# Kernel optimization log

Hardware: AMD Instinct MI355X
Metric: run time of the kernel (lower is better)

Reference implementation:

```python
import jax, jax.numpy as jnp
import numpy as np

H = 2048        # hidden_size
NH = 16         # num q heads
NKV = 4         # num kv heads
HD = 128        # head_dim
G = NH // NKV   # GQA group size
B = 32          # batch (decode sequences)
S = 4096        # max kv cache length per sequence
SCALE = HD ** -0.5
NEG = -1e30


def setup_inputs() -> dict:
    key = jax.random.key(0)
    ks = jax.random.split(key, 6)
    hidden_states = jax.random.normal(ks[0], (B, 1, H), dtype=jnp.float32)
    kv_cache = jax.random.normal(ks[1], (B, S, 2, NKV, HD), dtype=jnp.float32)
    seq_lens = jax.random.randint(ks[2], (B,), 1, S, dtype=jnp.int32)
    slot_mapping = seq_lens - 1  # write current token's k/v at its slot
    positions = (seq_lens - 1)[:, None].astype(jnp.int32)
    Wqkv = jax.random.normal(ks[3], (H, (NH + 2 * NKV) * HD), dtype=jnp.float32) * (H ** -0.5)
    bqkv = jax.random.normal(ks[4], ((NH + 2 * NKV) * HD,), dtype=jnp.float32) * 0.02
    Wo = jax.random.normal(ks[5], (NH * HD, H), dtype=jnp.float32) * ((NH * HD) ** -0.5)
    return {"hidden_states": hidden_states, "positions": positions, "kv_cache": kv_cache,
            "slot_mapping": slot_mapping, "seq_lens": seq_lens,
            "Wqkv": Wqkv, "bqkv": bqkv, "Wo": Wo}


def reference(hidden_states, positions, kv_cache, slot_mapping, seq_lens, Wqkv, bqkv, Wo):
    b, t, _ = hidden_states.shape  # t == 1 (decode)
    qkv = hidden_states.reshape(b * t, H) @ Wqkv + bqkv          # [B, (NH+2NKV)*HD]
    q, k, v = jnp.split(qkv, [NH * HD, (NH + NKV) * HD], axis=-1)
    q = q.reshape(b, NKV, G, HD)                                  # grouped-query layout
    k = k.reshape(b, NKV, HD)
    v = v.reshape(b, NKV, HD)
    # scatter current-step k/v into the paged cache at slot_mapping
    rows = jnp.arange(b)
    cache = kv_cache.at[rows, slot_mapping, 0].set(k)
    cache = cache.at[rows, slot_mapping, 1].set(v)
    keys = cache[:, :, 0]   # [B, S, NKV, HD]
    vals = cache[:, :, 1]   # [B, S, NKV, HD]
    # attention scores with ragged seq_lens mask
    scores = jnp.einsum('bkgd,bskd->bkgs', q, keys) * SCALE       # [B, NKV, G, S]
    valid = (jnp.arange(S)[None, :] < seq_lens[:, None])          # [B, S]
    scores = jnp.where(valid[:, None, None, :], scores, NEG)
    probs = jax.nn.softmax(scores, axis=-1)
    out = jnp.einsum('bkgs,bskd->bkgd', probs, vals)              # [B, NKV, G, HD]
    out = out.reshape(b * t, NH * HD)
    return (out @ Wo).reshape(b, t, H)
```

## Files before the change

### kernel.cpp

```cpp
#include <hip/hip_runtime.h>
#include <cstddef>

#define HQ 2048
#define NKVH 4
#define HDIM 128
#define QKV_N 3072
#define ATT_SCALE 0.08838834764831845f
#define KSPLIT 16
#define CHUNK 128
#define NCH 32

__device__ __forceinline__ float4 f4max(float4 a, float4 b) {
  return make_float4(fmaxf(a.x, b.x), fmaxf(a.y, b.y), fmaxf(a.z, b.z), fmaxf(a.w, b.w));
}

template <int N>
__global__ __launch_bounds__(256) void proj_kernel(const float* __restrict__ X,
                                                   const float* __restrict__ W,
                                                   float* __restrict__ part) {
  __shared__ union {
    float x[32][128];
    float red[32][4][64];
  } sm;
  const int t = threadIdx.x;
  const int c0 = blockIdx.x << 6;
  const int ksb = blockIdx.y;
  const int k0 = ksb << 7;
  const int c = t & 63;
  const int ksub = t >> 6;

#pragma unroll
  for (int i = 0; i < 4; ++i) {
    const int id = t + (i << 8);
    const int bb = id >> 5, kk = (id & 31) << 2;
    *reinterpret_cast<float4*>(&sm.x[bb][kk]) =
        *reinterpret_cast<const float4*>(X + bb * HQ + k0 + kk);
  }
  __syncthreads();

  float acc[32];
#pragma unroll
  for (int b = 0; b < 32; ++b) acc[b] = 0.f;

#pragma unroll
  for (int kk4 = 0; kk4 < 8; ++kk4) {
    const int kk = (ksub << 5) + (kk4 << 2);
    const float* wp = W + (size_t)(k0 + kk) * N + c0 + c;
    const float w0 = wp[0];
    const float w1 = wp[N];
    const float w2 = wp[2 * N];
    const float w3 = wp[3 * N];
#pragma unroll
    for (int b = 0; b < 32; ++b) {
      const float4 x4 = *reinterpret_cast<const float4*>(&sm.x[b][kk]);
      acc[b] = fmaf(x4.x, w0, acc[b]);
      acc[b] = fmaf(x4.y, w1, acc[b]);
      acc[b] = fmaf(x4.z, w2, acc[b]);
      acc[b] = fmaf(x4.w, w3, acc[b]);
    }
  }
  __syncthreads();
#pragma unroll
  for (int b = 0; b < 32; ++b) sm.red[b][ksub][c] = acc[b];
  __syncthreads();
#pragma unroll
  for (int i = 0; i < 8; ++i) {
    const int o = t + (i << 8);
    const int b = o >> 6, cc = o & 63;
    const float v = sm.red[b][0][cc] + sm.red[b][1][cc] + sm.red[b][2][cc] + sm.red[b][3][cc];
    part[(size_t)(ksb * 32 + b) * N + c0 + cc] = v;
  }
}

template <int NCOL, bool HAS_BIAS>
__global__ __launch_bounds__(256) void reduce_kernel(const float* __restrict__ part,
                                                     const float* __restrict__ bias,
                                                     float* __restrict__ out) {
  const int o = blockIdx.x * 256 + threadIdx.x;
  constexpr int total = 32 * NCOL;
  float s = 0.f;
#pragma unroll
  for (int ks = 0; ks < KSPLIT; ++ks) s += part[(size_t)ks * total + o];
  if (HAS_BIAS) s += bias[o % NCOL];
  out[o] = s;
}

__global__ __launch_bounds__(256, 2) void attn_kernel(const float* __restrict__ cache,
                                                      const int* __restrict__ seq_lens,
                                                      const int* __restrict__ slot_map,
                                                      const float* __restrict__ qkv,
                                                      float* __restrict__ ml,
                                                      float* __restrict__ accp) {
  __shared__ float pt[CHUNK][4];
  __shared__ float pvbuf[4][128][4];
  __shared__ float redm[4][4];
  __shared__ float redl[4][4];

  const int t = threadIdx.x;
  const int bid = blockIdx.x;
  const int chunk = bid & 31;
  const int kvh = (bid >> 5) & 3;
  const int b = bid >> 7;
  const int L = seq_lens[b];
  const int start = chunk << 7;
  if (start >= L) return;
  const int n = min(CHUNK, L - start);
  const int send = start + n;
  const int slot = slot_map[b];
  const float* __restrict__ qrow = qkv + b * QKV_N;
  const float* __restrict__ knew = qrow + 2048 + (kvh << 7);
  const float* __restrict__ vnew = qrow + 2560 + (kvh << 7);

  const int w = t >> 6, l = t & 63;
  const int l16 = l & 15, rq = l >> 4;
  const int wbase = w << 5;

  auto krow_ptr = [&](int r) -> const float* {
    int sg = start + r;
    sg = (sg < send) ? sg : start;
    return (sg == slot) ? knew : cache + (((size_t)((b << 12) + sg)) << 10) + (kvh << 7);
  };
  auto vrow_ptr = [&](int r) -> const float* {
    int sg = start + r;
    sg = (sg < send) ? sg : start;
    return (sg == slot) ? vnew : cache + (((size_t)((b << 12) + sg)) << 10) + 512 + (kvh << 7);
  };

  auto kload = [&](int st, float4* dst) {
#pragma unroll
    for (int rg = 0; rg < 4; ++rg) {
      const float* kp = krow_ptr(wbase + (st << 4) + (rg << 2) + rq) + (l16 << 3);
      dst[2 * rg] = *reinterpret_cast<const float4*>(kp);
      dst[2 * rg + 1] = *reinterpret_cast<const float4*>(kp + 4);
    }
  };
  auto vload = [&](int vt, float2* dst) {
#pragma unroll
    for (int s = 0; s < 16; ++s)
      dst[s] = *reinterpret_cast<const float2*>(vrow_ptr(wbase + (vt << 4) + s) + (l << 1));
  };

  float4 ka[8], kb[8];
  float2 va[16], vb[16];
  kload(0, ka);

  float4 qr[4][2];
#pragma unroll
  for (int g = 0; g < 4; ++g) {
#pragma unroll
    for (int e = 0; e < 2; ++e)
      qr[g][e] = *reinterpret_cast<const float4*>(qrow + ((kvh << 2) + g) * HDIM +
                                                  (l16 << 3) + (e << 2));
  }
  kload(1, kb);
  vload(0, va);
  vload(1, vb);

  float4 m4 = make_float4(-1e30f, -1e30f, -1e30f, -1e30f);
  auto score_st = [&](int st, const float4* kr) {
#pragma unroll
    for (int rg = 0; rg < 4; ++rg) {
      const float4 k0 = kr[2 * rg], k1 = kr[2 * rg + 1];
      float s0 = fmaf(k0.x, qr[0][0].x, fmaf(k0.y, qr[0][0].y, fmaf(k0.z, qr[0][0].z, k0.w * qr[0][0].w)));
      s0 = fmaf(k1.x, qr[0][1].x, fmaf(k1.y, qr[0][1].y, fmaf(k1.z, qr[0][1].z, fmaf(k1.w, qr[0][1].w, s0))));
      float s1 = fmaf(k0.x, qr[1][0].x, fmaf(k0.y, qr[1][0].y, fmaf(k0.z, qr[1][0].z, k0.w * qr[1][0].w)));
      s1 = fmaf(k1.x, qr[1][1].x, fmaf(k1.y, qr[1][1].y, fmaf(k1.z, qr[1][1].z, fmaf(k1.w, qr[1][1].w, s1))));
      float s2 = fmaf(k0.x, qr[2][0].x, fmaf(k0.y, qr[2][0].y, fmaf(k0.z, qr[2][0].z, k0.w * qr[2][0].w)));
      s2 = fmaf(k1.x, qr[2][1].x, fmaf(k1.y, qr[2][1].y, fmaf(k1.z, qr[2][1].z, fmaf(k1.w, qr[2][1].w, s2))));
      float s3 = fmaf(k0.x, qr[3][0].x, fmaf(k0.y, qr[3][0].y, fmaf(k0.z, qr[3][0].z, k0.w * qr[3][0].w)));
      s3 = fmaf(k1.x, qr[3][1].x, fmaf(k1.y, qr[3][1].y, fmaf(k1.z, qr[3][1].z, fmaf(k1.w, qr[3][1].w, s3))));
#pragma unroll
      for (int off = 1; off <= 8; off <<= 1) {
        s0 += __shfl_xor(s0, off);
        s1 += __shfl_xor(s1, off);
        s2 += __shfl_xor(s2, off);
        s3 += __shfl_xor(s3, off);
      }
      const int row = wbase + (st << 4) + (rg << 2) + rq;
      const float4 sc = make_float4(s0 * ATT_SCALE, s1 * ATT_SCALE, s2 * ATT_SCALE, s3 * ATT_SCALE);
      if (row < n) m4 = f4max(m4, sc);
      if (l16 == 0) *reinterpret_cast<float4*>(&pt[row][0]) = sc;
    }
  };

  score_st(0, ka);
  score_st(1, kb);

  m4.x = fmaxf(m4.x, __shfl_xor(m4.x, 16));
  m4.y = fmaxf(m4.y, __shfl_xor(m4.y, 16));
  m4.z = fmaxf(m4.z, __shfl_xor(m4.z, 16));
  m4.w = fmaxf(m4.w, __shfl_xor(m4.w, 16));
  m4.x = fmaxf(m4.x, __shfl_xor(m4.x, 32));
  m4.y = fmaxf(m4.y, __shfl_xor(m4.y, 32));
  m4.z = fmaxf(m4.z, __shfl_xor(m4.z, 32));
  m4.w = fmaxf(m4.w, __shfl_xor(m4.w, 32));
  if (l == 0) *reinterpret_cast<float4*>(&redm[w][0]) = m4;
  __syncthreads();
  float4 M4 = *reinterpret_cast<const float4*>(&redm[0][0]);
  M4 = f4max(M4, *reinterpret_cast<const float4*>(&redm[1][0]));
  M4 = f4max(M4, *reinterpret_cast<const float4*>(&redm[2][0]));
  M4 = f4max(M4, *reinterpret_cast<const float4*>(&redm[3][0]));

  float4 l4 = make_float4(0.f, 0.f, 0.f, 0.f);
  if (l < 32) {
    const int r = wbase + l;
    float4 e = make_float4(0.f, 0.f, 0.f, 0.f);
    if (r < n) {
      const float4 v = *reinterpret_cast<const float4*>(&pt[r][0]);
      e.x = __expf(v.x - M4.x);
      e.y = __expf(v.y - M4.y);
      e.z = __expf(v.z - M4.z);
      e.w = __expf(v.w - M4.w);
    }
    *reinterpret_cast<float4*>(&pt[r][0]) = e;
    l4 = e;
  }
#pragma unroll
  for (int off = 1; off <= 32; off <<= 1) {
    l4.x += __shfl_xor(l4.x, off);
    l4.y += __shfl_xor(l4.y, off);
    l4.z += __shfl_xor(l4.z, off);
    l4.w += __shfl_xor(l4.w, off);
  }
  if (l == 0) *reinterpret_cast<float4*>(&redl[w][0]) = l4;

  float4 accA = make_float4(0.f, 0.f, 0.f, 0.f);
  float4 accB = make_float4(0.f, 0.f, 0.f, 0.f);
#pragma unroll
  for (int s = 0; s < 16; ++s) {
    const float4 p = *reinterpret_cast<const float4*>(&pt[wbase + s][0]);
    const float2 vv = va[s];
    accA.x = fmaf(p.x, vv.x, accA.x); accA.y = fmaf(p.y, vv.x, accA.y);
    accA.z = fmaf(p.z, vv.x, accA.z); accA.w = fmaf(p.w, vv.x, accA.w);
    accB.x = fmaf(p.x, vv.y, accB.x); accB.y = fmaf(p.y, vv.y, accB.y);
    accB.z = fmaf(p.z, vv.y, accB.z); accB.w = fmaf(p.w, vv.y, accB.w);
  }
#pragma unroll
  for (int s = 0; s < 16; ++s) {
    const float4 p = *reinterpret_cast<const float4*>(&pt[wbase + 16 + s][0]);
    const float2 vv = vb[s];
    accA.x = fmaf(p.x, vv.x, accA.x); accA.y = fmaf(p.y, vv.x, accA.y);
    accA.z = fmaf(p.z, vv.x, accA.z); accA.w = fmaf(p.w, vv.x, accA.w);
    accB.x = fmaf(p.x, vv.y, accB.x); accB.y = fmaf(p.y, vv.y, accB.y);
    accB.z = fmaf(p.z, vv.y, accB.z); accB.w = fmaf(p.w, vv.y, accB.w);
  }

  *reinterpret_cast<float4*>(&pvbuf[w][l << 1][0]) = accA;
  *reinterpret_cast<float4*>(&pvbuf[w][(l << 1) + 1][0]) = accB;
  __syncthreads();

  if (t < 128) {
    const int d = t;
    float4 s0 = *reinterpret_cast<const float4*>(&pvbuf[0][d][0]);
    const float4 s1 = *reinterpret_cast<const float4*>(&pvbuf[1][d][0]);
    const float4 s2 = *reinterpret_cast<const float4*>(&pvbuf[2][d][0]);
    const float4 s3 = *reinterpret_cast<const float4*>(&pvbuf[3][d][0]);
    s0.x += s1.x + s2.x + s3.x;
    s0.y += s1.y + s2.y + s3.y;
    s0.z += s1.z + s2.z + s3.z;
    s0.w += s1.w + s2.w + s3.w;
    float* ap = accp + (size_t)bid * 512;
    ap[d] = s0.x;
    ap[128 + d] = s0.y;
    ap[256 + d] = s0.z;
    ap[384 + d] = s0.w;
  }
  if (t == 0) {
    float4 Lt = *reinterpret_cast<const float4*>(&redl[0][0]);
    const float4 l1 = *reinterpret_cast<const float4*>(&redl[1][0]);
    const float4 l2 = *reinterpret_cast<const float4*>(&redl[2][0]);
    const float4 l3 = *reinterpret_cast<const float4*>(&redl[3][0]);
    Lt.x += l1.x + l2.x + l3.x;
    Lt.y += l1.y + l2.y + l3.y;
    Lt.z += l1.z + l2.z + l3.z;
    Lt.w += l1.w + l2.w + l3.w;
    *reinterpret_cast<float4*>(ml + (size_t)bid * 8) = M4;
    *reinterpret_cast<float4*>(ml + (size_t)bid * 8 + 4) = Lt;
  }
}

__global__ __launch_bounds__(128) void combine_kernel(const int* __restrict__ seq_lens,
                                                      const float* __restrict__ ml,
                                                      const float* __restrict__ accp,
                                                      float* __restrict__ attn) {
  const int blk = blockIdx.x;
  const int g = blk & 3, kvh = (blk >> 2) & 3, b = blk >> 4;
  const int d = threadIdx.x;
  const int L = seq_lens[b];
  const int nch = (L + CHUNK - 1) >> 7;
  const int base = (b * 4 + kvh) * NCH;

  float M = -1e30f;
  for (int c = 0; c < nch; ++c) M = fmaxf(M, ml[(size_t)(base + c) * 8 + g]);
  float osum = 0.f, lsum = 0.f;
  for (int c = 0; c < nch; ++c) {
    const int idx = base + c;
    const float mc = ml[(size_t)idx * 8 + g];
    const float lc = ml[(size_t)idx * 8 + 4 + g];
    const float wgt = __expf(mc - M);
    lsum = fmaf(lc, wgt, lsum);
    osum = fmaf(wgt, accp[(size_t)idx * 512 + g * 128 + d], osum);
  }
  attn[(size_t)b * HQ + kvh * 512 + g * 128 + d] = osum / lsum;
}

extern "C" void kernel_launch(void* const* d_in, const int* in_sizes, int n_in,
                              void* d_out, int out_size, void* d_ws, size_t ws_size,
                              hipStream_t stream) {
  const float* hidden = (const float*)d_in[0];
  const float* cache = (const float*)d_in[2];
  const int* slot_map = (const int*)d_in[3];
  const int* seq_lens = (const int*)d_in[4];
  const float* Wqkv = (const float*)d_in[5];
  const float* bqkv = (const float*)d_in[6];
  const float* Wo = (const float*)d_in[7];
  float* out = (float*)d_out;
  float* ws = (float*)d_ws;

  float* qkv_part = ws;
  float* qkv      = ws + 1572864;
  float* ml       = ws + 1671168;
  float* accp     = ws + 1703936;
  float* attn     = ws + 3801088;
  float* o_part   = ws + 3866624;

  proj_kernel<QKV_N><<<dim3(48, KSPLIT), 256, 0, stream>>>(hidden, Wqkv, qkv_part);
  reduce_kernel<QKV_N, true><<<384, 256, 0, stream>>>(qkv_part, bqkv, qkv);
  attn_kernel<<<4096, 256, 0, stream>>>(cache, seq_lens, slot_map, qkv, ml, accp);
  combine_kernel<<<512, 128, 0, stream>>>(seq_lens, ml, accp, attn);
  proj_kernel<HQ><<<dim3(32, KSPLIT), 256, 0, stream>>>(attn, Wo, o_part);
  reduce_kernel<HQ, false><<<256, 256, 0, stream>>>(o_part, nullptr, out);
}
```

Baseline: 139.1 us.

## Split attention into score and PV kernels; widen projection tiles to 128 columns

The fused attention kernel is split into a score kernel, which writes scaled QK scores and per-wave maxima to workspace, and a PV kernel, which reads them back, applies exp and accumulates V. Each kernel holds fewer live registers (K or V only), so launch bounds are raised to 3 blocks per CU for higher occupancy. The extra score and max traffic through global memory, plus a second launch, is the price. Separately, the projection kernel now computes 128 columns per block with two accumulator sets, halving its grid and reusing the shared X tile across more weight columns.

```diff
diff --git a/kernel.cpp b/kernel.cpp
--- a/kernel.cpp
+++ b/kernel.cpp
@@ -23,7 +23,7 @@
     float red[32][4][64];
   } sm;
   const int t = threadIdx.x;
-  const int c0 = blockIdx.x << 6;
+  const int c0 = blockIdx.x << 7;
   const int ksb = blockIdx.y;
   const int k0 = ksb << 7;
   const int c = t & 63;
@@ -38,30 +38,35 @@
   }
   __syncthreads();
 
-  float acc[32];
-#pragma unroll
-  for (int b = 0; b < 32; ++b) acc[b] = 0.f;
+  float acc0[32], acc1[32];
+#pragma unroll
+  for (int b = 0; b < 32; ++b) { acc0[b] = 0.f; acc1[b] = 0.f; }
 
 #pragma unroll
   for (int kk4 = 0; kk4 < 8; ++kk4) {
     const int kk = (ksub << 5) + (kk4 << 2);
     const float* wp = W + (size_t)(k0 + kk) * N + c0 + c;
-    const float w0 = wp[0];
-    const float w1 = wp[N];
-    const float w2 = wp[2 * N];
-    const float w3 = wp[3 * N];
+    const float w0a = wp[0],     w0b = wp[64];
+    const float w1a = wp[N],     w1b = wp[N + 64];
+    const float w2a = wp[2 * N], w2b = wp[2 * N + 64];
+    const float w3a = wp[3 * N], w3b = wp[3 * N + 64];
 #pragma unroll
     for (int b = 0; b < 32; ++b) {
       const float4 x4 = *reinterpret_cast<const float4*>(&sm.x[b][kk]);
-      acc[b] = fmaf(x4.x, w0, acc[b]);
-      acc[b] = fmaf(x4.y, w1, acc[b]);
-      acc[b] = fmaf(x4.z, w2, acc[b]);
-      acc[b] = fmaf(x4.w, w3, acc[b]);
+      acc0[b] = fmaf(x4.x, w0a, acc0[b]);
+      acc0[b] = fmaf(x4.y, w1a, acc0[b]);
+      acc0[b] = fmaf(x4.z, w2a, acc0[b]);
+      acc0[b] = fmaf(x4.w, w3a, acc0[b]);
+      acc1[b] = fmaf(x4.x, w0b, acc1[b]);
+      acc1[b] = fmaf(x4.y, w1b, acc1[b]);
+      acc1[b] = fmaf(x4.z, w2b, acc1[b]);
+      acc1[b] = fmaf(x4.w, w3b, acc1[b]);
     }
   }
-  __syncthreads();
-#pragma unroll
-  for (int b = 0; b < 32; ++b) sm.red[b][ksub][c] = acc[b];
+
+  __syncthreads();
+#pragma unroll
+  for (int b = 0; b < 32; ++b) sm.red[b][ksub][c] = acc0[b];
   __syncthreads();
 #pragma unroll
   for (int i = 0; i < 8; ++i) {
@@ -69,6 +74,17 @@
     const int b = o >> 6, cc = o & 63;
     const float v = sm.red[b][0][cc] + sm.red[b][1][cc] + sm.red[b][2][cc] + sm.red[b][3][cc];
     part[(size_t)(ksb * 32 + b) * N + c0 + cc] = v;
+  }
+  __syncthreads();
+#pragma unroll
+  for (int b = 0; b < 32; ++b) sm.red[b][ksub][c] = acc1[b];
+  __syncthreads();
+#pragma unroll
+  for (int i = 0; i < 8; ++i) {
+    const int o = t + (i << 8);
+    const int b = o >> 6, cc = o & 63;
+    const float v = sm.red[b][0][cc] + sm.red[b][1][cc] + sm.red[b][2][cc] + sm.red[b][3][cc];
+    part[(size_t)(ksb * 32 + b) * N + c0 + 64 + cc] = v;
   }
 }
 
@@ -85,17 +101,12 @@
   out[o] = s;
 }
 
-__global__ __launch_bounds__(256, 2) void attn_kernel(const float* __restrict__ cache,
-                                                      const int* __restrict__ seq_lens,
-                                                      const int* __restrict__ slot_map,
-                                                      const float* __restrict__ qkv,
-                                                      float* __restrict__ ml,
-                                                      float* __restrict__ accp) {
-  __shared__ float pt[CHUNK][4];
-  __shared__ float pvbuf[4][128][4];
-  __shared__ float redm[4][4];
-  __shared__ float redl[4][4];
-
+__global__ __launch_bounds__(256, 3) void score_kernel(const float* __restrict__ cache,
+                                                       const int* __restrict__ seq_lens,
+                                                       const int* __restrict__ slot_map,
+                                                       const float* __restrict__ qkv,
+                                                       float* __restrict__ scores,
+                                                       float* __restrict__ wmax) {
   const int t = threadIdx.x;
   const int bid = blockIdx.x;
   const int chunk = bid & 31;
@@ -109,23 +120,25 @@
   const int slot = slot_map[b];
   const float* __restrict__ qrow = qkv + b * QKV_N;
   const float* __restrict__ knew = qrow + 2048 + (kvh << 7);
-  const float* __restrict__ vnew = qrow + 2560 + (kvh << 7);
 
   const int w = t >> 6, l = t & 63;
   const int l16 = l & 15, rq = l >> 4;
   const int wbase = w << 5;
+
+  float4 qr[4][2];
+#pragma unroll
+  for (int g = 0; g < 4; ++g) {
+#pragma unroll
+    for (int e = 0; e < 2; ++e)
+      qr[g][e] = *reinterpret_cast<const float4*>(qrow + ((kvh << 2) + g) * HDIM +
+                                                  (l16 << 3) + (e << 2));
+  }
 
   auto krow_ptr = [&](int r) -> const float* {
     int sg = start + r;
     sg = (sg < send) ? sg : start;
     return (sg == slot) ? knew : cache + (((size_t)((b << 12) + sg)) << 10) + (kvh << 7);
   };
-  auto vrow_ptr = [&](int r) -> const float* {
-    int sg = start + r;
-    sg = (sg < send) ? sg : start;
-    return (sg == slot) ? vnew : cache + (((size_t)((b << 12) + sg)) << 10) + 512 + (kvh << 7);
-  };
-
   auto kload = [&](int st, float4* dst) {
 #pragma unroll
     for (int rg = 0; rg < 4; ++rg) {
@@ -134,27 +147,10 @@
       dst[2 * rg + 1] = *reinterpret_cast<const float4*>(kp + 4);
     }
   };
-  auto vload = [&](int vt, float2* dst) {
-#pragma unroll
-    for (int s = 0; s < 16; ++s)
-      dst[s] = *reinterpret_cast<const float2*>(vrow_ptr(wbase + (vt << 4) + s) + (l << 1));
-  };
 
   float4 ka[8], kb[8];
-  float2 va[16], vb[16];
   kload(0, ka);
-
-  float4 qr[4][2];
-#pragma unroll
-  for (int g = 0; g < 4; ++g) {
-#pragma unroll
-    for (int e = 0; e < 2; ++e)
-      qr[g][e] = *reinterpret_cast<const float4*>(qrow + ((kvh << 2) + g) * HDIM +
-                                                  (l16 << 3) + (e << 2));
-  }
   kload(1, kb);
-  vload(0, va);
-  vload(1, vb);
 
   float4 m4 = make_float4(-1e30f, -1e30f, -1e30f, -1e30f);
   auto score_st = [&](int st, const float4* kr) {
@@ -179,7 +175,8 @@
       const int row = wbase + (st << 4) + (rg << 2) + rq;
       const float4 sc = make_float4(s0 * ATT_SCALE, s1 * ATT_SCALE, s2 * ATT_SCALE, s3 * ATT_SCALE);
       if (row < n) m4 = f4max(m4, sc);
-      if (l16 == 0) *reinterpret_cast<float4*>(&pt[row][0]) = sc;
+      if (l16 == 0)
+        *reinterpret_cast<float4*>(scores + ((size_t)bid << 9) + (row << 2)) = sc;
     }
   };
 
@@ -194,27 +191,69 @@
   m4.y = fmaxf(m4.y, __shfl_xor(m4.y, 32));
   m4.z = fmaxf(m4.z, __shfl_xor(m4.z, 32));
   m4.w = fmaxf(m4.w, __shfl_xor(m4.w, 32));
-  if (l == 0) *reinterpret_cast<float4*>(&redm[w][0]) = m4;
-  __syncthreads();
-  float4 M4 = *reinterpret_cast<const float4*>(&redm[0][0]);
-  M4 = f4max(M4, *reinterpret_cast<const float4*>(&redm[1][0]));
-  M4 = f4max(M4, *reinterpret_cast<const float4*>(&redm[2][0]));
-  M4 = f4max(M4, *reinterpret_cast<const float4*>(&redm[3][0]));
-
-  float4 l4 = make_float4(0.f, 0.f, 0.f, 0.f);
-  if (l < 32) {
-    const int r = wbase + l;
-    float4 e = make_float4(0.f, 0.f, 0.f, 0.f);
-    if (r < n) {
-      const float4 v = *reinterpret_cast<const float4*>(&pt[r][0]);
-      e.x = __expf(v.x - M4.x);
-      e.y = __expf(v.y - M4.y);
-      e.z = __expf(v.z - M4.z);
-      e.w = __expf(v.w - M4.w);
-    }
-    *reinterpret_cast<float4*>(&pt[r][0]) = e;
-    l4 = e;
-  }
+  if (l == 0) *reinterpret_cast<float4*>(wmax + (bid << 4) + (w << 2)) = m4;
+}
+
+__global__ __launch_bounds__(256, 3) void pv_kernel(const float* __restrict__ cache,
+                                                    const int* __restrict__ seq_lens,
+                                                    const int* __restrict__ slot_map,
+                                                    const float* __restrict__ qkv,
+                                                    const float* __restrict__ scores,
+                                                    const float* __restrict__ wmax,
+                                                    float* __restrict__ ml,
+                                                    float* __restrict__ accp) {
+  __shared__ float pt[4][32][4];
+  __shared__ float pvbuf[4][128][4];
+  __shared__ float redl[4][4];
+
+  const int t = threadIdx.x;
+  const int bid = blockIdx.x;
+  const int chunk = bid & 31;
+  const int kvh = (bid >> 5) & 3;
+  const int b = bid >> 7;
+  const int L = seq_lens[b];
+  const int start = chunk << 7;
+  if (start >= L) return;
+  const int n = min(CHUNK, L - start);
+  const int send = start + n;
+  const int slot = slot_map[b];
+  const float* __restrict__ vnew = qkv + b * QKV_N + 2560 + (kvh << 7);
+
+  const int w = t >> 6, l = t & 63;
+  const int wbase = w << 5;
+
+  auto vrow_ptr = [&](int r) -> const float* {
+    int sg = start + r;
+    sg = (sg < send) ? sg : start;
+    return (sg == slot) ? vnew : cache + (((size_t)((b << 12) + sg)) << 10) + 512 + (kvh << 7);
+  };
+  auto vload = [&](int vt, float2* dst) {
+#pragma unroll
+    for (int s = 0; s < 16; ++s)
+      dst[s] = *reinterpret_cast<const float2*>(vrow_ptr(wbase + (vt << 4) + s) + (l << 1));
+  };
+
+  const float4 wm0 = *reinterpret_cast<const float4*>(wmax + (bid << 4));
+  const float4 wm1 = *reinterpret_cast<const float4*>(wmax + (bid << 4) + 4);
+  const float4 wm2 = *reinterpret_cast<const float4*>(wmax + (bid << 4) + 8);
+  const float4 wm3 = *reinterpret_cast<const float4*>(wmax + (bid << 4) + 12);
+  float4 s4 = make_float4(0.f, 0.f, 0.f, 0.f);
+  if (l < 32)
+    s4 = *reinterpret_cast<const float4*>(scores + ((size_t)bid << 9) + ((wbase + l) << 2));
+  float2 va[16], vb[16];
+  vload(0, va);
+  vload(1, vb);
+
+  const float4 M4 = f4max(f4max(wm0, wm1), f4max(wm2, wm3));
+  float4 e = make_float4(0.f, 0.f, 0.f, 0.f);
+  if (l < 32 && wbase + l < n) {
+    e.x = __expf(s4.x - M4.x);
+    e.y = __expf(s4.y - M4.y);
+    e.z = __expf(s4.z - M4.z);
+    e.w = __expf(s4.w - M4.w);
+  }
+  if (l < 32) *reinterpret_cast<float4*>(&pt[w][l][0]) = e;
+  float4 l4 = e;
 #pragma unroll
   for (int off = 1; off <= 32; off <<= 1) {
     l4.x += __shfl_xor(l4.x, off);
@@ -223,12 +262,13 @@
     l4.w += __shfl_xor(l4.w, off);
   }
   if (l == 0) *reinterpret_cast<float4*>(&redl[w][0]) = l4;
+  asm volatile("s_waitcnt lgkmcnt(0)" ::: "memory");
 
   float4 accA = make_float4(0.f, 0.f, 0.f, 0.f);
   float4 accB = make_float4(0.f, 0.f, 0.f, 0.f);
 #pragma unroll
   for (int s = 0; s < 16; ++s) {
-    const float4 p = *reinterpret_cast<const float4*>(&pt[wbase + s][0]);
+    const float4 p = *reinterpret_cast<const float4*>(&pt[w][s][0]);
     const float2 vv = va[s];
     accA.x = fmaf(p.x, vv.x, accA.x); accA.y = fmaf(p.y, vv.x, accA.y);
     accA.z = fmaf(p.z, vv.x, accA.z); accA.w = fmaf(p.w, vv.x, accA.w);
@@ -237,7 +277,7 @@
   }
 #pragma unroll
   for (int s = 0; s < 16; ++s) {
-    const float4 p = *reinterpret_cast<const float4*>(&pt[wbase + 16 + s][0]);
+    const float4 p = *reinterpret_cast<const float4*>(&pt[w][16 + s][0]);
     const float2 vv = vb[s];
     accA.x = fmaf(p.x, vv.x, accA.x); accA.y = fmaf(p.y, vv.x, accA.y);
     accA.z = fmaf(p.z, vv.x, accA.z); accA.w = fmaf(p.w, vv.x, accA.w);
@@ -323,11 +363,14 @@
   float* accp     = ws + 1703936;
   float* attn     = ws + 3801088;
   float* o_part   = ws + 3866624;
-
-  proj_kernel<QKV_N><<<dim3(48, KSPLIT), 256, 0, stream>>>(hidden, Wqkv, qkv_part);
+  float* scores   = ws + 4915200;
+  float* wmax     = ws + 7012352;
+
+  proj_kernel<QKV_N><<<dim3(24, KSPLIT), 256, 0, stream>>>(hidden, Wqkv, qkv_part);
   reduce_kernel<QKV_N, true><<<384, 256, 0, stream>>>(qkv_part, bqkv, qkv);
-  attn_kernel<<<4096, 256, 0, stream>>>(cache, seq_lens, slot_map, qkv, ml, accp);
+  score_kernel<<<4096, 256, 0, stream>>>(cache, seq_lens, slot_map, qkv, scores, wmax);
+  pv_kernel<<<4096, 256, 0, stream>>>(cache, seq_lens, slot_map, qkv, scores, wmax, ml, accp);
   combine_kernel<<<512, 128, 0, stream>>>(seq_lens, ml, accp, attn);
-  proj_kernel<HQ><<<dim3(32, KSPLIT), 256, 0, stream>>>(attn, Wo, o_part);
+  proj_kernel<HQ><<<dim3(16, KSPLIT), 256, 0, stream>>>(attn, Wo, o_part);
   reduce_kernel<HQ, false><<<256, 256, 0, stream>>>(o_part, nullptr, out);
 }
```

Result: slower. 149.5 us (+7.5%).
